# Kernel optimization log

Hardware: AMD Instinct MI355X
Metric: run time of the kernel (lower is better)

## Reference

```python
import jax, jax.numpy as jnp
import numpy as np

B, T, N, U = 64, 128, 128, 128  # batch, seq_len, n_features, lstm units


def setup_inputs() -> dict:
    key = jax.random.key(0)
    ks = jax.random.split(key, 8)
    s = 0.05
    return {
        "x": jax.random.normal(ks[0], (B, T, N), dtype=jnp.float32),
        "hidden_state": jnp.zeros((B, U), jnp.float32),
        "cell_state": jnp.zeros((B, U), jnp.float32),
        "lstm_kernel": jax.random.normal(ks[1], (N, 4 * U), jnp.float32) * s,
        "lstm_bias": jnp.zeros((4 * U,), jnp.float32),
        "w1_kernel": jax.random.normal(ks[2], (1, T), jnp.float32) * s,
        "w1_bias": jnp.zeros((T,), jnp.float32),
        "w2_kernel": jax.random.normal(ks[3], (2 * U, T), jnp.float32) * s,
        "w2_bias": jnp.zeros((T,), jnp.float32),
        "v_kernel": jax.random.normal(ks[4], (T, 1), jnp.float32) * s,
        "v_bias": jnp.zeros((1,), jnp.float32),
        "n": N,
    }


def reference(x, hidden_state, cell_state, lstm_kernel, lstm_bias,
              w1_kernel, w1_bias, w2_kernel, w2_bias, v_kernel, v_bias, n):
    # NewLSTM ignores the provided initial state, so every timestep's LSTM
    # runs a length-1 sequence from zero (h, c). No recurrence -> vectorize
    # over time. Keras gate order: i, f, c(g), o; recurrent kernel * 0 drops out.
    z = x @ lstm_kernel + lstm_bias                       # (B,T,4U)
    i, f, g, o = jnp.split(z, 4, axis=-1)
    c = jax.nn.sigmoid(i) * jnp.tanh(g)                   # f-gate * c_prev(=0) vanishes
    h = jax.nn.sigmoid(o) * jnp.tanh(c)                   # (B,T,U)

    # Input attention per timestep, vectorized over T.
    query = jnp.concatenate([h, c], axis=-1)              # (B,T,2U)
    s2 = query @ w2_kernel + w2_bias                      # (B,T,T)
    # w1 is Dense(T) on a size-1 feature axis: x_scalar * w1_kernel[0] + b.
    s1 = x[..., None] * w1_kernel[0] + w1_bias            # (B,T,N,T)
    score = jnp.tanh(s1 + s2[:, :, None, :])              # (B,T,N,T)
    e = jnp.einsum('btnk,k->btn', score, v_kernel[:, 0]) + v_bias[0]  # (B,T,N)
    alpha = jax.nn.softmax(e, axis=-1)                    # softmax over features

    return x * alpha                                      # (B,T,N)
```

## Files before the change

kernel.cpp:

```cpp
#include <hip/hip_runtime.h>
#include <math.h>


typedef __attribute__((ext_vector_type(8))) short short8;
typedef __attribute__((ext_vector_type(4))) float f32x4;

#define BT 8192
#define NF 128
#define K_C     2.8853900817779268f
#define K_LOG2E 1.4426950408889634f

__device__ __forceinline__ float fast_rcp(float x)  { return __builtin_amdgcn_rcpf(x); }
__device__ __forceinline__ float fast_exp2(float x) { return __builtin_amdgcn_exp2f(x); }

__device__ __forceinline__ float tanh_from_scaled(float tC) {
    float e = fast_exp2(fabsf(tC));
    float r = fmaf(-2.f, fast_rcp(1.f + e), 1.f);
    return copysignf(r, tC);
}
__device__ __forceinline__ float tanh_fast(float t) { return tanh_from_scaled(t * K_C); }
__device__ __forceinline__ float sig_fast(float z) {
    return fast_rcp(1.f + fast_exp2(-K_LOG2E * z));
}
__device__ __forceinline__ unsigned short f2bf(float f) {
    unsigned u = __float_as_uint(f);
    return (unsigned short)((u + 0x7fffu + ((u >> 16) & 1u)) >> 16);
}

__global__ __launch_bounds__(64) void prep(const float* __restrict__ Wl,
                                           const float* __restrict__ w2,
                                           unsigned short* __restrict__ wsB) {
    const int lane = threadIdx.x;
    const int n16 = lane & 15, q = lane >> 4;
    const int b = blockIdx.x;
    if (b < 96) {
        const int nt = b >> 2, kk = b & 3;
        const int g = nt >> 3, jt = nt & 7;
        const int goff = (g == 0) ? 0 : (g == 1 ? 256 : 384);
        const int col = goff + jt * 16 + n16;
        unsigned short* d = wsB + b * 512 + lane * 8;
        #pragma unroll
        for (int j = 0; j < 8; j++)
            d[j] = f2bf(Wl[(kk * 32 + q * 8 + j) * 512 + col]);
    } else {
        const int fs = b - 96;
        const int nt2 = fs >> 3, kk2 = fs & 7;
        const int col = nt2 * 16 + n16;
        unsigned short* d = wsB + 49152 + fs * 512 + lane * 8;
        #pragma unroll
        for (int j = 0; j < 8; j++)
            d[j] = f2bf(w2[(kk2 * 32 + q * 8 + j) * 128 + col]);
    }
}

__global__ __launch_bounds__(256, 3) void g1(
    const float* __restrict__ x,  const unsigned short* __restrict__ wsB,
    const float* __restrict__ bl, const float* __restrict__ b2,
    const float* __restrict__ b1, float* __restrict__ s2c)
{
    __shared__ unsigned short B1s[24 * 512];
    __shared__ unsigned short Qf[2 * 4096];
    const int t    = threadIdx.x;
    const int lane = t & 63, w = t >> 6;
    const int n16  = lane & 15, q = lane >> 4;
    const int mt   = w & 1, js = w >> 1;
    const int rowbase = blockIdx.x * 32 + mt * 16;

    short8 af[4];
    const float* xrow = x + (rowbase + n16) * 128 + q * 8;
    #pragma unroll
    for (int kk = 0; kk < 4; kk++) {
        const float4 v0 = *(const float4*)(xrow + kk * 32);
        const float4 v1 = *(const float4*)(xrow + kk * 32 + 4);
        short8 a;
        a[0] = f2bf(v0.x); a[1] = f2bf(v0.y); a[2] = f2bf(v0.z); a[3] = f2bf(v0.w);
        a[4] = f2bf(v1.x); a[5] = f2bf(v1.y); a[6] = f2bf(v1.z); a[7] = f2bf(v1.w);
        af[kk] = a;
    }

    f32x4 acc[4][3];
    #pragma unroll
    for (int tr = 0; tr < 4; tr++)
        #pragma unroll
        for (int g = 0; g < 3; g++) acc[tr][g] = (f32x4)(0.f);

    const uint4* Bg = (const uint4*)wsB;
    for (int ph = 0; ph < 4; ph++) {
        __syncthreads();
        for (int i = t; i < 1536; i += 256) {
            const int nt = i >> 6;
            ((uint4*)B1s)[i] = Bg[(nt * 4 + ph) * 64 + (i & 63)];
        }
        __syncthreads();
        #pragma unroll
        for (int tr = 0; tr < 4; tr++) {
            const int jt = js * 4 + tr;
            #pragma unroll
            for (int g = 0; g < 3; g++) {
                const short8 bf = *(const short8*)&B1s[(g * 8 + jt) * 512 + lane * 8];
                acc[tr][g] = __builtin_amdgcn_mfma_f32_16x16x32_bf16(
                    af[ph], bf, acc[tr][g], 0, 0, 0);
            }
        }
    }

    #pragma unroll
    for (int tr = 0; tr < 4; tr++) {
        const int jt = js * 4 + tr;
        const int u  = jt * 16 + n16;
        const float bi = bl[u], bg = bl[256 + u], bo = bl[384 + u];
        const int kqh = u, kqc = 128 + u;
        const int baseh = mt * 4096 + (kqh >> 5) * 512 + ((kqh & 31) >> 3) * 128
                        + q * 32 + (kqh & 7);
        const int basec = mt * 4096 + (kqc >> 5) * 512 + ((kqc & 31) >> 3) * 128
                        + q * 32 + (kqc & 7);
        #pragma unroll
        for (int r = 0; r < 4; r++) {
            const float c = sig_fast(acc[tr][0][r] + bi) * tanh_fast(acc[tr][1][r] + bg);
            const float h = sig_fast(acc[tr][2][r] + bo) * tanh_fast(c);
            Qf[baseh + r * 8] = f2bf(h);
            Qf[basec + r * 8] = f2bf(c);
        }
    }
    __syncthreads();

    short8 a2[8];
    #pragma unroll
    for (int kk2 = 0; kk2 < 8; kk2++)
        a2[kk2] = *(const short8*)&Qf[mt * 4096 + kk2 * 512 + lane * 8];

    const short8* B2g = (const short8*)(wsB + 49152);
    #pragma unroll
    for (int tr2 = 0; tr2 < 4; tr2++) {
        const int nt2 = js * 4 + tr2;
        f32x4 acc2 = (f32x4)(0.f);
        #pragma unroll
        for (int kk2 = 0; kk2 < 8; kk2++) {
            const short8 bf = B2g[(nt2 * 8 + kk2) * 64 + lane];
            acc2 = __builtin_amdgcn_mfma_f32_16x16x32_bf16(a2[kk2], bf, acc2, 0, 0, 0);
        }
        const int u2 = nt2 * 16 + n16;
        const float bias2 = (b2[u2] + b1[u2]) * K_C;
        #pragma unroll
        for (int r = 0; r < 4; r++)
            s2c[(rowbase + q * 4 + r) * 128 + u2] = fmaf(acc2[r], K_C, bias2);
    }
}

__global__ __launch_bounds__(128) void phase2(
    const float* __restrict__ x,  const float* __restrict__ w1,
    const float* __restrict__ v,  const float* __restrict__ s2c,
    float* __restrict__ out)
{
    __shared__ __align__(16) float w1Cs[NF];
    __shared__ __align__(16) float vs[NF];
    __shared__ __align__(16) float c2s[NF];
    __shared__ __align__(16) float part[4][32];
    __shared__ float Ftab[32];
    __shared__ float red[4];
    const int t   = threadIdx.x;
    const int row = blockIdx.x;

    w1Cs[t] = w1[t] * K_C;
    vs[t]   = v[t];
    c2s[t]  = s2c[row * NF + t];
    const float xn = x[row * NF + t];

    float mn = xn, mx = xn;
    #pragma unroll
    for (int off = 1; off < 64; off <<= 1) {
        mn = fminf(mn, __shfl_xor(mn, off, 64));
        mx = fmaxf(mx, __shfl_xor(mx, off, 64));
    }
    if ((t & 63) == 0) { red[t >> 6] = mn; red[2 + (t >> 6)] = mx; }
    __syncthreads();
    mn = fminf(red[0], red[1]);
    mx = fmaxf(red[2], red[3]);
    const float span = mx - mn;
    const float h    = span * (1.f / 29.f);
    const float invh = span > 1e-12f ? 29.f / span : 0.f;

    const int   m  = t & 31, qq = t >> 5;
    const float xi = fmaf((float)(m - 1), h, mn);
    float acc = 0.f;
    const int k0 = qq * 32;
    #pragma unroll
    for (int j = 0; j < 32; j += 4) {
        const float4 w4 = *(const float4*)&w1Cs[k0 + j];
        const float4 c4 = *(const float4*)&c2s[k0 + j];
        const float4 v4 = *(const float4*)&vs[k0 + j];
        acc = fmaf(tanh_from_scaled(fmaf(xi, w4.x, c4.x)), v4.x, acc);
        acc = fmaf(tanh_from_scaled(fmaf(xi, w4.y, c4.y)), v4.y, acc);
        acc = fmaf(tanh_from_scaled(fmaf(xi, w4.z, c4.z)), v4.z, acc);
        acc = fmaf(tanh_from_scaled(fmaf(xi, w4.w, c4.w)), v4.w, acc);
    }
    part[qq][m] = acc;
    __syncthreads();
    if (t < 32) Ftab[t] = (part[0][t] + part[1][t]) + (part[2][t] + part[3][t]);
    __syncthreads();

    float sN = fmaf(xn - mn, invh, 1.0f);
    int   i  = (int)sN;
    i = i < 1 ? 1 : (i > 29 ? 29 : i);
    const float f  = sN - (float)i;
    const float F0 = Ftab[i - 1], F1 = Ftab[i], F2 = Ftab[i + 1], F3 = Ftab[i + 2];
    const float e  = F1 + 0.5f * f * ((F2 - F0)
                   + f * ((2.f * F0 - 5.f * F1 + 4.f * F2 - F3)
                   + f * (3.f * (F1 - F2) + F3 - F0)));

    float mval = e;
    #pragma unroll
    for (int off = 1; off < 64; off <<= 1) mval = fmaxf(mval, __shfl_xor(mval, off, 64));
    if ((t & 63) == 0) red[t >> 6] = mval;
    __syncthreads();
    mval = fmaxf(red[0], red[1]);
    const float p = fast_exp2(K_LOG2E * (e - mval));
    float ssum = p;
    #pragma unroll
    for (int off = 1; off < 64; off <<= 1) ssum += __shfl_xor(ssum, off, 64);
    if ((t & 63) == 0) red[2 + (t >> 6)] = ssum;
    __syncthreads();
    ssum = red[2] + red[3];

    out[row * NF + t] = xn * p * fast_rcp(ssum);
}

extern "C" void kernel_launch(void* const* d_in, const int* in_sizes, int n_in,
                              void* d_out, int out_size, void* d_ws, size_t ws_size,
                              hipStream_t stream) {
    const float* x  = (const float*)d_in[0];
    const float* Wl = (const float*)d_in[3];
    const float* bl = (const float*)d_in[4];
    const float* w1 = (const float*)d_in[5];
    const float* b1 = (const float*)d_in[6];
    const float* w2 = (const float*)d_in[7];
    const float* b2 = (const float*)d_in[8];
    const float* v  = (const float*)d_in[9];
    float* out = (float*)d_out;

    unsigned short* wsB = (unsigned short*)d_ws;
    const size_t wreq = 160 * 1024;
    float* s2c = (ws_size >= wreq + (size_t)BT * NF * sizeof(float))
               ? (float*)((char*)d_ws + wreq) : out;

    prep<<<160, 64, 0, stream>>>(Wl, w2, wsB);
    g1<<<256, 256, 0, stream>>>(x, wsB, bl, b2, b1, s2c);
    phase2<<<BT, 128, 0, stream>>>(x, w1, v, s2c, out);
}
```

Measured before the change: 104.7 us.

## Fuse LSTM/score GEMMs with attention softmax into one per-16-row kernel

Merges the GEMM kernel and the per-row attention kernel into a single kernel that handles 16 rows per block. The s2 scores stay in shared memory instead of being written to global workspace and read back. The 30-point interpolation table, the min/max reductions and the softmax are all computed per row inside that block. B fragments are now read straight from global memory instead of being staged through LDS. The tanh helper drops its abs/copysign steps, and the kernel also gives up some of the old occupancy hint and the per-block data reuse the 32-row tile provided.

Measured after the change: 94.54 us. 1.11x faster.

```diff
diff --git a/kernel.cpp b/kernel.cpp
--- a/kernel.cpp
+++ b/kernel.cpp
@@ -13,12 +13,10 @@
 __device__ __forceinline__ float fast_rcp(float x)  { return __builtin_amdgcn_rcpf(x); }
 __device__ __forceinline__ float fast_exp2(float x) { return __builtin_amdgcn_exp2f(x); }
 
-__device__ __forceinline__ float tanh_from_scaled(float tC) {
-    float e = fast_exp2(fabsf(tC));
-    float r = fmaf(-2.f, fast_rcp(1.f + e), 1.f);
-    return copysignf(r, tC);
-}
-__device__ __forceinline__ float tanh_fast(float t) { return tanh_from_scaled(t * K_C); }
+__device__ __forceinline__ float tanh_nc(float tC) {
+    return fmaf(-2.f, fast_rcp(1.f + fast_exp2(tC)), 1.f);
+}
+__device__ __forceinline__ float tanh_fast(float t) { return tanh_nc(t * K_C); }
 __device__ __forceinline__ float sig_fast(float z) {
     return fast_rcp(1.f + fast_exp2(-K_LOG2E * z));
 }
@@ -53,21 +51,30 @@
     }
 }
 
-__global__ __launch_bounds__(256, 3) void g1(
+__global__ __launch_bounds__(256, 2) void enc(
     const float* __restrict__ x,  const unsigned short* __restrict__ wsB,
     const float* __restrict__ bl, const float* __restrict__ b2,
-    const float* __restrict__ b1, float* __restrict__ s2c)
+    const float* __restrict__ b1, const float* __restrict__ w1,
+    const float* __restrict__ v,  float* __restrict__ out)
 {
-    __shared__ unsigned short B1s[24 * 512];
-    __shared__ unsigned short Qf[2 * 4096];
+    __shared__ __align__(16) float xs[16][NF];
+    __shared__ unsigned short Qf[8 * 512];
+    __shared__ __align__(16) float c2[16][NF];
+    __shared__ __align__(16) float w1Cs[NF], vs[NF];
+    __shared__ float Ftab[16][32];
+    __shared__ float rowMn[16], rowMx[16];
+
     const int t    = threadIdx.x;
     const int lane = t & 63, w = t >> 6;
     const int n16  = lane & 15, q = lane >> 4;
-    const int mt   = w & 1, js = w >> 1;
-    const int rowbase = blockIdx.x * 32 + mt * 16;
+    const int rowbase = blockIdx.x * 16;
+
+    for (int i = t; i < 512; i += 256)
+        ((float4*)xs)[i] = ((const float4*)(x + rowbase * NF))[i];
+    if (t < NF) { w1Cs[t] = w1[t] * K_C; vs[t] = v[t]; }
 
     short8 af[4];
-    const float* xrow = x + (rowbase + n16) * 128 + q * 8;
+    const float* xrow = x + (rowbase + n16) * NF + q * 8;
     #pragma unroll
     for (int kk = 0; kk < 4; kk++) {
         const float4 v0 = *(const float4*)(xrow + kk * 32);
@@ -78,46 +85,37 @@
         af[kk] = a;
     }
 
-    f32x4 acc[4][3];
-    #pragma unroll
-    for (int tr = 0; tr < 4; tr++)
-        #pragma unroll
-        for (int g = 0; g < 3; g++) acc[tr][g] = (f32x4)(0.f);
-
-    const uint4* Bg = (const uint4*)wsB;
-    for (int ph = 0; ph < 4; ph++) {
-        __syncthreads();
-        for (int i = t; i < 1536; i += 256) {
-            const int nt = i >> 6;
-            ((uint4*)B1s)[i] = Bg[(nt * 4 + ph) * 64 + (i & 63)];
-        }
-        __syncthreads();
-        #pragma unroll
-        for (int tr = 0; tr < 4; tr++) {
-            const int jt = js * 4 + tr;
+    f32x4 acc[2][3];
+    #pragma unroll
+    for (int j2 = 0; j2 < 2; j2++)
+        #pragma unroll
+        for (int g = 0; g < 3; g++) acc[j2][g] = (f32x4)(0.f);
+    const short8* B1g = (const short8*)wsB;
+    #pragma unroll
+    for (int kk = 0; kk < 4; kk++)
+        #pragma unroll
+        for (int j2 = 0; j2 < 2; j2++) {
+            const int jt = w * 2 + j2;
             #pragma unroll
             for (int g = 0; g < 3; g++) {
-                const short8 bf = *(const short8*)&B1s[(g * 8 + jt) * 512 + lane * 8];
-                acc[tr][g] = __builtin_amdgcn_mfma_f32_16x16x32_bf16(
-                    af[ph], bf, acc[tr][g], 0, 0, 0);
+                const short8 bf = B1g[(((g * 8 + jt) * 4) + kk) * 64 + lane];
+                acc[j2][g] = __builtin_amdgcn_mfma_f32_16x16x32_bf16(
+                    af[kk], bf, acc[j2][g], 0, 0, 0);
             }
         }
-    }
-
-    #pragma unroll
-    for (int tr = 0; tr < 4; tr++) {
-        const int jt = js * 4 + tr;
+
+    #pragma unroll
+    for (int j2 = 0; j2 < 2; j2++) {
+        const int jt = w * 2 + j2;
         const int u  = jt * 16 + n16;
         const float bi = bl[u], bg = bl[256 + u], bo = bl[384 + u];
-        const int kqh = u, kqc = 128 + u;
-        const int baseh = mt * 4096 + (kqh >> 5) * 512 + ((kqh & 31) >> 3) * 128
-                        + q * 32 + (kqh & 7);
-        const int basec = mt * 4096 + (kqc >> 5) * 512 + ((kqc & 31) >> 3) * 128
-                        + q * 32 + (kqc & 7);
+        const int kqh = u, kqc = NF + u;
+        const int baseh = (kqh >> 5) * 512 + ((kqh & 31) >> 3) * 128 + q * 32 + (kqh & 7);
+        const int basec = (kqc >> 5) * 512 + ((kqc & 31) >> 3) * 128 + q * 32 + (kqc & 7);
         #pragma unroll
         for (int r = 0; r < 4; r++) {
-            const float c = sig_fast(acc[tr][0][r] + bi) * tanh_fast(acc[tr][1][r] + bg);
-            const float h = sig_fast(acc[tr][2][r] + bo) * tanh_fast(c);
+            const float c = sig_fast(acc[j2][0][r] + bi) * tanh_fast(acc[j2][1][r] + bg);
+            const float h = sig_fast(acc[j2][2][r] + bo) * tanh_fast(c);
             Qf[baseh + r * 8] = f2bf(h);
             Qf[basec + r * 8] = f2bf(c);
         }
@@ -127,12 +125,11 @@
     short8 a2[8];
     #pragma unroll
     for (int kk2 = 0; kk2 < 8; kk2++)
-        a2[kk2] = *(const short8*)&Qf[mt * 4096 + kk2 * 512 + lane * 8];
-
+        a2[kk2] = *(const short8*)&Qf[kk2 * 512 + lane * 8];
     const short8* B2g = (const short8*)(wsB + 49152);
     #pragma unroll
-    for (int tr2 = 0; tr2 < 4; tr2++) {
-        const int nt2 = js * 4 + tr2;
+    for (int j2 = 0; j2 < 2; j2++) {
+        const int nt2 = w * 2 + j2;
         f32x4 acc2 = (f32x4)(0.f);
         #pragma unroll
         for (int kk2 = 0; kk2 < 8; kk2++) {
@@ -143,86 +140,86 @@
         const float bias2 = (b2[u2] + b1[u2]) * K_C;
         #pragma unroll
         for (int r = 0; r < 4; r++)
-            s2c[(rowbase + q * 4 + r) * 128 + u2] = fmaf(acc2[r], K_C, bias2);
-    }
-}
-
-__global__ __launch_bounds__(128) void phase2(
-    const float* __restrict__ x,  const float* __restrict__ w1,
-    const float* __restrict__ v,  const float* __restrict__ s2c,
-    float* __restrict__ out)
-{
-    __shared__ __align__(16) float w1Cs[NF];
-    __shared__ __align__(16) float vs[NF];
-    __shared__ __align__(16) float c2s[NF];
-    __shared__ __align__(16) float part[4][32];
-    __shared__ float Ftab[32];
-    __shared__ float red[4];
-    const int t   = threadIdx.x;
-    const int row = blockIdx.x;
-
-    w1Cs[t] = w1[t] * K_C;
-    vs[t]   = v[t];
-    c2s[t]  = s2c[row * NF + t];
-    const float xn = x[row * NF + t];
-
-    float mn = xn, mx = xn;
-    #pragma unroll
-    for (int off = 1; off < 64; off <<= 1) {
-        mn = fminf(mn, __shfl_xor(mn, off, 64));
-        mx = fmaxf(mx, __shfl_xor(mx, off, 64));
-    }
-    if ((t & 63) == 0) { red[t >> 6] = mn; red[2 + (t >> 6)] = mx; }
+            c2[q * 4 + r][u2] = fmaf(acc2[r], K_C, bias2);
+    }
+
+    #pragma unroll
+    for (int r4 = 0; r4 < 4; r4++) {
+        const int row = w * 4 + r4;
+        float a = xs[row][lane], b = xs[row][64 + lane];
+        float mn = fminf(a, b), mx = fmaxf(a, b);
+        #pragma unroll
+        for (int off = 1; off < 64; off <<= 1) {
+            mn = fminf(mn, __shfl_xor(mn, off, 64));
+            mx = fmaxf(mx, __shfl_xor(mx, off, 64));
+        }
+        if (lane == 0) { rowMn[row] = mn; rowMx[row] = mx; }
+    }
     __syncthreads();
-    mn = fminf(red[0], red[1]);
-    mx = fmaxf(red[2], red[3]);
-    const float span = mx - mn;
-    const float h    = span * (1.f / 29.f);
-    const float invh = span > 1e-12f ? 29.f / span : 0.f;
-
-    const int   m  = t & 31, qq = t >> 5;
-    const float xi = fmaf((float)(m - 1), h, mn);
-    float acc = 0.f;
-    const int k0 = qq * 32;
-    #pragma unroll
-    for (int j = 0; j < 32; j += 4) {
-        const float4 w4 = *(const float4*)&w1Cs[k0 + j];
-        const float4 c4 = *(const float4*)&c2s[k0 + j];
-        const float4 v4 = *(const float4*)&vs[k0 + j];
-        acc = fmaf(tanh_from_scaled(fmaf(xi, w4.x, c4.x)), v4.x, acc);
-        acc = fmaf(tanh_from_scaled(fmaf(xi, w4.y, c4.y)), v4.y, acc);
-        acc = fmaf(tanh_from_scaled(fmaf(xi, w4.z, c4.z)), v4.z, acc);
-        acc = fmaf(tanh_from_scaled(fmaf(xi, w4.w, c4.w)), v4.w, acc);
-    }
-    part[qq][m] = acc;
+
+    #pragma unroll
+    for (int p = 0; p < 2; p++) {
+        const int row = p * 8 + (t >> 5);
+        const int m   = t & 31;
+        const float mn = rowMn[row];
+        const float h  = (rowMx[row] - mn) * (1.f / 29.f);
+        const float xi = fmaf((float)(m - 1), h, mn);
+        float accF = 0.f;
+        #pragma unroll 4
+        for (int k = 0; k < NF; k += 4) {
+            const float4 w4 = *(const float4*)&w1Cs[k];
+            const float4 c4 = *(const float4*)&c2[row][k];
+            const float4 v4 = *(const float4*)&vs[k];
+            accF = fmaf(tanh_nc(fmaf(xi, w4.x, c4.x)), v4.x, accF);
+            accF = fmaf(tanh_nc(fmaf(xi, w4.y, c4.y)), v4.y, accF);
+            accF = fmaf(tanh_nc(fmaf(xi, w4.z, c4.z)), v4.z, accF);
+            accF = fmaf(tanh_nc(fmaf(xi, w4.w, c4.w)), v4.w, accF);
+        }
+        Ftab[row][m] = accF;
+    }
     __syncthreads();
-    if (t < 32) Ftab[t] = (part[0][t] + part[1][t]) + (part[2][t] + part[3][t]);
-    __syncthreads();
-
-    float sN = fmaf(xn - mn, invh, 1.0f);
-    int   i  = (int)sN;
-    i = i < 1 ? 1 : (i > 29 ? 29 : i);
-    const float f  = sN - (float)i;
-    const float F0 = Ftab[i - 1], F1 = Ftab[i], F2 = Ftab[i + 1], F3 = Ftab[i + 2];
-    const float e  = F1 + 0.5f * f * ((F2 - F0)
-                   + f * ((2.f * F0 - 5.f * F1 + 4.f * F2 - F3)
-                   + f * (3.f * (F1 - F2) + F3 - F0)));
-
-    float mval = e;
-    #pragma unroll
-    for (int off = 1; off < 64; off <<= 1) mval = fmaxf(mval, __shfl_xor(mval, off, 64));
-    if ((t & 63) == 0) red[t >> 6] = mval;
-    __syncthreads();
-    mval = fmaxf(red[0], red[1]);
-    const float p = fast_exp2(K_LOG2E * (e - mval));
-    float ssum = p;
-    #pragma unroll
-    for (int off = 1; off < 64; off <<= 1) ssum += __shfl_xor(ssum, off, 64);
-    if ((t & 63) == 0) red[2 + (t >> 6)] = ssum;
-    __syncthreads();
-    ssum = red[2] + red[3];
-
-    out[row * NF + t] = xn * p * fast_rcp(ssum);
+
+    {
+        const int row = t >> 4;
+        const int n0  = (t & 15) * 8;
+        const float mn   = rowMn[row];
+        const float span = rowMx[row] - mn;
+        const float invh = span > 1e-12f ? 29.f / span : 0.f;
+        float xv[8], e8[8];
+        *(float4*)&xv[0] = *(const float4*)&xs[row][n0];
+        *(float4*)&xv[4] = *(const float4*)&xs[row][n0 + 4];
+        #pragma unroll
+        for (int i = 0; i < 8; i++) {
+            const float sN = fmaf(xv[i] - mn, invh, 1.0f);
+            int ii = (int)sN;
+            ii = ii < 1 ? 1 : (ii > 29 ? 29 : ii);
+            const float f  = sN - (float)ii;
+            const float F0 = Ftab[row][ii - 1], F1 = Ftab[row][ii];
+            const float F2 = Ftab[row][ii + 1], F3 = Ftab[row][ii + 2];
+            e8[i] = F1 + 0.5f * f * ((F2 - F0)
+                  + f * ((2.f * F0 - 5.f * F1 + 4.f * F2 - F3)
+                  + f * (3.f * (F1 - F2) + F3 - F0)));
+        }
+        float mval = e8[0];
+        #pragma unroll
+        for (int i = 1; i < 8; i++) mval = fmaxf(mval, e8[i]);
+        #pragma unroll
+        for (int off = 1; off < 16; off <<= 1) mval = fmaxf(mval, __shfl_xor(mval, off, 64));
+        float ssum = 0.f;
+        #pragma unroll
+        for (int i = 0; i < 8; i++) { e8[i] = fast_exp2(K_LOG2E * (e8[i] - mval)); ssum += e8[i]; }
+        #pragma unroll
+        for (int off = 1; off < 16; off <<= 1) ssum += __shfl_xor(ssum, off, 64);
+        const float rs = fast_rcp(ssum);
+        float4 o0, o1;
+        o0.x = xv[0] * e8[0] * rs; o0.y = xv[1] * e8[1] * rs;
+        o0.z = xv[2] * e8[2] * rs; o0.w = xv[3] * e8[3] * rs;
+        o1.x = xv[4] * e8[4] * rs; o1.y = xv[5] * e8[5] * rs;
+        o1.z = xv[6] * e8[6] * rs; o1.w = xv[7] * e8[7] * rs;
+        float* op = out + (rowbase + row) * NF + n0;
+        *(float4*)op       = o0;
+        *(float4*)(op + 4) = o1;
+    }
 }
 
 extern "C" void kernel_launch(void* const* d_in, const int* in_sizes, int n_in,
@@ -237,13 +234,8 @@
     const float* b2 = (const float*)d_in[8];
     const float* v  = (const float*)d_in[9];
     float* out = (float*)d_out;
-
     unsigned short* wsB = (unsigned short*)d_ws;
-    const size_t wreq = 160 * 1024;
-    float* s2c = (ws_size >= wreq + (size_t)BT * NF * sizeof(float))
-               ? (float*)((char*)d_ws + wreq) : out;
 
     prep<<<160, 64, 0, stream>>>(Wl, w2, wsB);
-    g1<<<256, 256, 0, stream>>>(x, wsB, bl, b2, b1, s2c);
-    phase2<<<BT, 128, 0, stream>>>(x, w1, v, s2c, out);
-}
+    enc<<<BT / 16, 256, 0, stream>>>(x, wsB, bl, b2, b1, w1, v, out);
+}
```
